# Kernel tuning notes

Measured on AMD Instinct MI355X. Metric: run time of the kernel, lower is better.

The kernel has to match this reference:

```python
import jax, jax.numpy as jnp
import numpy as np

EMB = 1024; H = 8; HD = EMB // H // 2  # head_dim = 64, q/k use 2*H heads of HD; v uses H heads of 2*HD
FF = 4096; DEPTH = 1
LAM_INIT = float(0.8 - 0.6 * np.exp(-0.3 * DEPTH))

def setup_inputs() -> dict:
    key = jax.random.key(0)
    ks = jax.random.split(key, 12)
    s = lambda k, sh, sc: jax.random.normal(k, sh, jnp.float32) * sc
    return {
        'x': s(ks[0], (2, 2048, EMB), 1.0),
        'ln1_w': jnp.ones((EMB,), jnp.float32), 'ln1_b': jnp.zeros((EMB,), jnp.float32),
        'Wq': s(ks[1], (EMB, EMB), 0.02), 'Wk': s(ks[2], (EMB, EMB), 0.02),
        'Wv': s(ks[3], (EMB, EMB), 0.02), 'Wo': s(ks[4], (EMB, EMB), 0.02),
        'lq1': s(ks[5], (HD,), 0.1), 'lk1': s(ks[6], (HD,), 0.1),
        'lq2': s(ks[7], (HD,), 0.1), 'lk2': s(ks[8], (HD,), 0.1),
        'subln_w': jnp.ones((2 * HD,), jnp.float32),
        'ln2_w': jnp.ones((EMB,), jnp.float32), 'ln2_b': jnp.zeros((EMB,), jnp.float32),
        'W1': s(ks[9], (EMB, FF), 0.02), 'b1': jnp.zeros((FF,), jnp.float32),
        'W2': s(ks[10], (FF, EMB), 0.02), 'b2': jnp.zeros((EMB,), jnp.float32),
    }

def _ln(x, w, b):
    m = jnp.mean(x, -1, keepdims=True)
    v = jnp.var(x, -1, keepdims=True)
    return (x - m) * jax.lax.rsqrt(v + 1e-5) * w + b

def _rms(x, w):
    return x * jax.lax.rsqrt(jnp.mean(x * x, -1, keepdims=True) + 1e-5) * w

def reference(x, ln1_w, ln1_b, Wq, Wk, Wv, Wo, lq1, lk1, lq2, lk2, subln_w, ln2_w, ln2_b, W1, b1, W2, b2):
    B, N, _ = x.shape
    h = _ln(x, ln1_w, ln1_b)
    q = (h @ Wq).reshape(B, N, 2 * H, HD) * (HD ** -0.5)
    k = (h @ Wk).reshape(B, N, 2 * H, HD)
    v = (h @ Wv).reshape(B, N, H, 2 * HD)
    # dual softmax attention maps: [B, 2H, N, N]
    attn = jax.nn.softmax(jnp.einsum('bihd,bjhd->bhij', q, k), axis=-1)
    attn = attn.reshape(B, H, 2, N, N)
    lam = jnp.exp(jnp.sum(lq1 * lk1)) - jnp.exp(jnp.sum(lq2 * lk2)) + LAM_INIT
    a = attn[:, :, 0] - lam * attn[:, :, 1]  # differential attention [B,H,N,N]
    o = jnp.einsum('bhij,bjhd->bihd', a, v)  # [B,N,H,2*HD]
    o = _rms(o, subln_w) * (1.0 - LAM_INIT)
    x = x + o.reshape(B, N, EMB) @ Wo
    h = _ln(x, ln2_w, ln2_b)
    return x + (jax.nn.gelu(h @ W1 + b1, approximate=False) @ W2 + b2)
```

## Files before the change

### kernel.cpp

```cpp
#include <hip/hip_runtime.h>


typedef unsigned short u16;
typedef unsigned int u32;
typedef __attribute__((ext_vector_type(8))) __bf16 bf16x8;
typedef __attribute__((ext_vector_type(4))) float f32x4;
typedef __attribute__((ext_vector_type(4))) u32 u32x4;
typedef __attribute__((ext_vector_type(2))) u32 u32x2;

#define LOG2E 1.4426950408889634f
#define LAM_INIT 0.355509068f
#define ONE_MINUS_LAM_INIT 0.644490932f

__device__ __forceinline__ float bf2f(u16 x) {
  u32 u = ((u32)x) << 16;
  return __builtin_bit_cast(float, u);
}
__device__ __forceinline__ u16 f2bf(float f) {
  u32 u = __builtin_bit_cast(u32, f);
  u32 r = (u + 0x7FFFu + ((u >> 16) & 1u)) >> 16;
  return (u16)r;
}
__device__ __forceinline__ u32 cvtpk(float lo, float hi) {
  u32 r;
  asm("v_cvt_pk_bf16_f32 %0, %1, %2" : "=v"(r) : "v"(lo), "v"(hi));
  return r;
}
__device__ __forceinline__ float ldf(const void* p, size_t i, bool f32) {
  return f32 ? ((const float*)p)[i] : bf2f(((const u16*)p)[i]);
}
__device__ __forceinline__ void async16(const u16* g, u16* l) {
  __builtin_amdgcn_global_load_lds((const __attribute__((address_space(1))) u32*)g,
                                   (__attribute__((address_space(3))) u32*)l, 16, 0, 0);
}
__device__ __forceinline__ bf16x8 ld8(const u16* p) { return *(const bf16x8*)p; }

__global__ void detect_kernel(const u32* x, int* flag) {
  int e = (x[threadIdx.x] >> 7) & 0xFF;
  unsigned long long m = __ballot(e >= 90 && e <= 150);
  if (threadIdx.x == 0) flag[0] = (__popcll(m) >= 40) ? 1 : 0;
}

__global__ void lam_kernel(const void* lq1, const void* lk1, const void* lq2,
                           const void* lk2, const int* flag, float* out) {
  const bool f32 = flag[0] == 0;
  int L = threadIdx.x;
  float a = ldf(lq1, L, f32) * ldf(lk1, L, f32);
  float c = ldf(lq2, L, f32) * ldf(lk2, L, f32);
#pragma unroll
  for (int m = 1; m < 64; m <<= 1) { a += __shfl_xor(a, m); c += __shfl_xor(c, m); }
  if (L == 0) out[0] = __expf(a) - __expf(c) + LAM_INIT;
}

__device__ __forceinline__ void unpack8(u32x4 u, float* f) {
#pragma unroll
  for (int i = 0; i < 4; ++i) {
    f[2 * i] = bf2f((u16)(u[i] & 0xffffu));
    f[2 * i + 1] = bf2f((u16)(u[i] >> 16));
  }
}

template <bool XRAW>
__global__ __launch_bounds__(256) void ln_kernel(const void* __restrict__ x,
                                                 const void* __restrict__ w,
                                                 const void* __restrict__ b,
                                                 const int* __restrict__ flag,
                                                 u16* __restrict__ out) {
  const bool f32 = flag[0] == 0;
  const int row = blockIdx.x * 4 + (threadIdx.x >> 6);
  const int L = threadIdx.x & 63;
  float xv[16];
  if (XRAW && f32) {
    const f32x4* xr = (const f32x4*)((const float*)x + (size_t)row * 1024 + L * 16);
#pragma unroll
    for (int i = 0; i < 4; ++i) {
      f32x4 vv = xr[i];
#pragma unroll
      for (int j = 0; j < 4; ++j) xv[i * 4 + j] = vv[j];
    }
  } else {
    const u16* xr = (const u16*)x + (size_t)row * 1024 + L * 16;
    unpack8(*(const u32x4*)xr, xv);
    unpack8(*(const u32x4*)(xr + 8), xv + 8);
  }
  float s = 0.f, sq = 0.f;
#pragma unroll
  for (int i = 0; i < 16; ++i) { s += xv[i]; sq += xv[i] * xv[i]; }
#pragma unroll
  for (int m = 1; m < 64; m <<= 1) { s += __shfl_xor(s, m); sq += __shfl_xor(sq, m); }
  float mean = s * (1.0f / 1024.0f);
  float var = sq * (1.0f / 1024.0f) - mean * mean;
  float rstd = rsqrtf(var + 1e-5f);
  u32 pk[8];
#pragma unroll
  for (int i = 0; i < 8; ++i) {
    float w0 = ldf(w, L * 16 + 2 * i, f32), w1 = ldf(w, L * 16 + 2 * i + 1, f32);
    float b0 = ldf(b, L * 16 + 2 * i, f32), b1v = ldf(b, L * 16 + 2 * i + 1, f32);
    float v0 = (xv[2 * i] - mean) * rstd * w0 + b0;
    float v1 = (xv[2 * i + 1] - mean) * rstd * w1 + b1v;
    pk[i] = (u32)f2bf(v0) | ((u32)f2bf(v1) << 16);
  }
  u32x4 o0 = {pk[0], pk[1], pk[2], pk[3]};
  u32x4 o1 = {pk[4], pk[5], pk[6], pk[7]};
  *(u32x4*)(out + (size_t)row * 1024 + L * 16) = o0;
  *(u32x4*)(out + (size_t)row * 1024 + L * 16 + 8) = o1;
}

__global__ __launch_bounds__(256) void twc_kernel(const void* __restrict__ s0,
                                                  const void* __restrict__ s1,
                                                  const void* __restrict__ s2,
                                                  u16* __restrict__ dst, int sstride,
                                                  int dstride, size_t soff, size_t dzoff,
                                                  const int* __restrict__ flag) {
  __shared__ __align__(16) u16 tile[64][72];
  const bool f32 = flag[0] == 0;
  const void* src = blockIdx.z == 0 ? s0 : (blockIdx.z == 1 ? s1 : s2);
  u16* dz = dst + (size_t)blockIdx.z * dzoff;
  const int r0 = blockIdx.y * 64, c0 = blockIdx.x * 64;
  const int t = threadIdx.x;
  const int rr = t >> 3, cc = t & 7;
#pragma unroll
  for (int i = 0; i < 2; ++i) {
    int row = rr + i * 32;
    size_t idx = (size_t)(r0 + row) * sstride + c0 + cc * 8 + soff;
    if (f32) {
      const f32x4* s = (const f32x4*)((const float*)src + idx);
      f32x4 a = s[0], b = s[1];
      union { u16 t16[8]; u32x4 v; } u_;
#pragma unroll
      for (int j = 0; j < 4; ++j) { u_.t16[j] = f2bf(a[j]); u_.t16[4 + j] = f2bf(b[j]); }
      *(u32x4*)(&tile[row][cc * 8]) = u_.v;
    } else {
      *(u32x4*)(&tile[row][cc * 8]) = *(const u32x4*)((const u16*)src + idx);
    }
  }
  __syncthreads();
  u16* d = dz + (size_t)c0 * dstride + r0;
#pragma unroll
  for (int i = 0; i < 2; ++i) {
    int n = rr + i * 32;
    union { u16 t16[8]; u32x4 v; } u_;
#pragma unroll
    for (int j = 0; j < 8; ++j) u_.t16[j] = tile[cc * 8 + j][n];
    *(u32x4*)(d + (size_t)n * dstride + cc * 8) = u_.v;
  }
}

enum { EP_NONE = 0, EP_RES = 2, EP_GELU = 3, EP_BIASRES = 4, EP_QKV = 5 };

template <int TM, int EPI, bool RESRAW, bool OUTFLEX, bool DB>
__global__ __launch_bounds__(256, 2) void gemm_bt(
    const u16* __restrict__ A, const u16* __restrict__ Bt, void* __restrict__ Cv,
    int M, int N, int K, const void* __restrict__ bias, int boff,
    const void* __restrict__ res, const int* __restrict__ flag,
    u16* __restrict__ kout, u16* __restrict__ vtout) {
  constexpr int MT = TM / 32;
  constexpr int HALF = TM * 64 + 128 * 64;
  extern __shared__ __align__(16) u16 lds[];
  const int t = threadIdx.x;
  const int w = t >> 6, L = t & 63;
  const int quad = L >> 4, l16 = L & 15;
  const int m0 = blockIdx.y * TM, n0 = blockIdx.x * 128;
  const int wm = (TM == 128) ? (w >> 1) * 64 : (w & 1) * 32;
  const int wn = (TM == 128) ? (w & 1) * 64 : (w >> 1) * 64;
  const int srow = L >> 3, spc = L & 7;
  const int sc = spc ^ srow;

  f32x4 acc[MT][4] = {};
  const u16* Ab = A + (size_t)m0 * K;
  const u16* Bb = Bt + (size_t)n0 * K;

  auto stage = [&](int kt, int bsel) {
    u16* base = lds + bsel * HALF;
#pragma unroll
    for (int r = 0; r < TM / 32; ++r) {
      int row = r * 32 + w * 8 + srow;
      async16(Ab + (size_t)row * K + kt + sc * 8, &base[row * 64 + spc * 8]);
    }
#pragma unroll
    for (int r = 0; r < 4; ++r) {
      int row = r * 32 + w * 8 + srow;
      async16(Bb + (size_t)row * K + kt + sc * 8, &base[TM * 64 + row * 64 + spc * 8]);
    }
  };
  auto ktile = [&](const u16* base) {
#pragma unroll
    for (int ks = 0; ks < 2; ++ks) {
      bf16x8 af[MT], bfr[4];
#pragma unroll
      for (int mt = 0; mt < MT; ++mt) {
        int row = wm + mt * 16 + l16;
        af[mt] = ld8(&base[row * 64 + (((ks * 4 + quad) ^ (l16 & 7)) * 8)]);
      }
#pragma unroll
      for (int nt = 0; nt < 4; ++nt) {
        int row = wn + nt * 16 + l16;
        bfr[nt] = ld8(&base[TM * 64 + row * 64 + (((ks * 4 + quad) ^ (l16 & 7)) * 8)]);
      }
#pragma unroll
      for (int mt = 0; mt < MT; ++mt)
#pragma unroll
        for (int nt = 0; nt < 4; ++nt)
          acc[mt][nt] =
              __builtin_amdgcn_mfma_f32_16x16x32_bf16(af[mt], bfr[nt], acc[mt][nt], 0, 0, 0);
    }
  };

  if (DB) {
    const int nst = K >> 6;
    stage(0, 0);
    for (int st = 0; st < nst; ++st) {
      __syncthreads();
      if (st + 1 < nst) stage((st + 1) << 6, (st + 1) & 1);
      ktile(lds + (st & 1) * HALF);
    }
  } else {
    for (int kt = 0; kt < K; kt += 64) {
      stage(kt, 0);
      __syncthreads();
      ktile(lds);
      __syncthreads();
    }
  }

  const bool f32 = flag[0] == 0;
#pragma unroll
  for (int mt = 0; mt < MT; ++mt) {
#pragma unroll
    for (int nt = 0; nt < 4; ++nt) {
      int col = n0 + wn + nt * 16 + l16;
      float bv = 0.f;
      if (EPI == EP_GELU || EPI == EP_BIASRES) bv = ldf(bias, (size_t)boff + col, f32);
#pragma unroll
      for (int r = 0; r < 4; ++r) {
        int row = m0 + wm + mt * 16 + quad * 4 + r;
        float v = acc[mt][nt][r];
        if (EPI == EP_GELU) {
          v += bv;
          v = 0.5f * v * (1.0f + erff(v * 0.70710678118654752f));
        }
        if (EPI == EP_RES || EPI == EP_BIASRES) {
          size_t ri = (size_t)row * N + col;
          float rv = RESRAW ? ldf(res, ri, f32) : bf2f(((const u16*)res)[ri]);
          v += rv;
          if (EPI == EP_BIASRES) v += bv;
        }
        if (EPI == EP_QKV) {
          if (col < 1024) {
            ((u16*)Cv)[(size_t)row * 1024 + col] = f2bf(v * 0.125f);
          } else if (col < 2048) {
            kout[(size_t)row * 1024 + (col - 1024)] = f2bf(v);
          } else {
            int c2 = col - 2048;
            int bb = row >> 11, n = row & 2047, hh = c2 >> 7, d = c2 & 127;
            vtout[(size_t)((bb * 8 + hh) * 128 + d) * 2048 + n] = f2bf(v);
          }
        } else {
          size_t ci = (size_t)row * N + col;
          if (OUTFLEX && f32)
            ((float*)Cv)[ci] = v;
          else
            ((u16*)Cv)[ci] = f2bf(v);
        }
      }
    }
  }
}

__global__ __launch_bounds__(256, 2) void attn_kernel(
    const u16* __restrict__ q, const u16* __restrict__ k, const u16* __restrict__ vT,
    const float* __restrict__ lamp, const void* __restrict__ subw,
    const int* __restrict__ flag, u16* __restrict__ o) {
  extern __shared__ __align__(16) u16 lds[];
  constexpr int VB = 16384, PB = 32768;
  const int t = threadIdx.x, w = t >> 6, L = t & 63;
  const int quad = L >> 4, l16 = L & 15;
  const int bid = ((blockIdx.x & 7) << 6) | (blockIdx.x >> 3);
  const int qt = bid & 31, h = (bid >> 5) & 7, b = bid >> 8;
  const int q0 = qt * 64;
  const int comp = w >> 1, rh = (w & 1) * 32;
  const int srow = L >> 3, spc = L & 7, sc = spc ^ srow;
  const u16* vb = vT + (size_t)(b * 8 + h) * (128 * 2048);
  const int pbase = PB + w * 2048;

  auto stageK = [&](int kt, int bsel) {
#pragma unroll
    for (int r = 0; r < 4; ++r) {
      int row = r * 32 + w * 8 + srow;
      int c_ = row >> 6, key = row & 63;
      async16(k + ((size_t)(b * 2048 + kt + key) * 1024 + (2 * h + c_) * 64 + sc * 8),
              &lds[bsel * 8192 + row * 64 + spc * 8]);
    }
  };
  auto stageV = [&](int kt, int bsel) {
#pragma unroll
    for (int r = 0; r < 4; ++r) {
      int dim = r * 32 + w * 8 + srow;
      async16(vb + (size_t)dim * 2048 + kt + sc * 8,
              &lds[VB + bsel * 8192 + dim * 64 + spc * 8]);
    }
  };

  stageK(0, 0);
  stageV(0, 0);
#pragma unroll
  for (int r = 0; r < 4; ++r) {
    int row = r * 32 + w * 8 + srow;
    int c_ = row >> 6, qr = row & 63;
    async16(q + ((size_t)(b * 2048 + q0 + qr) * 1024 + (2 * h + c_) * 64 + sc * 8),
            &lds[PB + row * 64 + spc * 8]);
  }
  __syncthreads();
  bf16x8 qf[2][2];
#pragma unroll
  for (int mt = 0; mt < 2; ++mt)
#pragma unroll
    for (int ks = 0; ks < 2; ++ks) {
      int row = rh + mt * 16 + l16;
      qf[mt][ks] =
          ld8(&lds[PB + comp * 4096 + row * 64 + (((ks * 4 + quad) ^ (l16 & 7)) * 8)]);
    }

  float mst[2] = {-1.0e30f, -1.0e30f};
  float mstl[2] = {-1.0e30f, -1.0e30f};
  float lst[2] = {0.f, 0.f};
  f32x4 oacc[8][2] = {};

  for (int ti = 0; ti < 32; ++ti) {
    __syncthreads();
    const int bb = ti & 1;
    if (ti + 1 < 32) {
      stageK((ti + 1) * 64, bb ^ 1);
      stageV((ti + 1) * 64, bb ^ 1);
    }

    f32x4 s[4][2] = {};
#pragma unroll
    for (int ks = 0; ks < 2; ++ks) {
      bf16x8 kf[4];
#pragma unroll
      for (int nt = 0; nt < 4; ++nt) {
        int row = nt * 16 + l16;
        kf[nt] = ld8(&lds[bb * 8192 + comp * 4096 + row * 64 +
                          (((ks * 4 + quad) ^ (l16 & 7)) * 8)]);
      }
#pragma unroll
      for (int nt = 0; nt < 4; ++nt)
#pragma unroll
        for (int mt = 0; mt < 2; ++mt)
          s[nt][mt] = __builtin_amdgcn_mfma_f32_16x16x32_bf16(kf[nt], qf[mt][ks], s[nt][mt], 0, 0, 0);
    }

#pragma unroll
    for (int mt = 0; mt < 2; ++mt) {
      float mx = -3.0e38f;
#pragma unroll
      for (int nt = 0; nt < 4; ++nt)
#pragma unroll
        for (int r = 0; r < 4; ++r) mx = fmaxf(mx, s[nt][mt][r]);
      mx = fmaxf(mx, __shfl_xor(mx, 16));
      mx = fmaxf(mx, __shfl_xor(mx, 32));
      if (__ballot(mx > mst[mt] + 8.0f)) {
        float mnew = fmaxf(mst[mt], mx);
        float al = exp2f((mst[mt] - mnew) * LOG2E);
        mst[mt] = mnew;
        mstl[mt] = mnew * LOG2E;
        lst[mt] *= al;
#pragma unroll
        for (int nt = 0; nt < 8; ++nt)
#pragma unroll
          for (int r = 0; r < 4; ++r) oacc[nt][mt][r] *= al;
      }
      float ps = 0.f;
#pragma unroll
      for (int nt = 0; nt < 4; ++nt)
#pragma unroll
        for (int r = 0; r < 4; ++r) {
          float p = exp2f(__builtin_fmaf(s[nt][mt][r], LOG2E, -mstl[mt]));
          s[nt][mt][r] = p;
          ps += p;
        }
      ps += __shfl_xor(ps, 16);
      ps += __shfl_xor(ps, 32);
      lst[mt] += ps;
    }

#pragma unroll
    for (int mt = 0; mt < 2; ++mt) {
      int prow = mt * 16 + l16;
#pragma unroll
      for (int nt = 0; nt < 4; ++nt) {
        int pc = (nt * 2 + (quad >> 1)) ^ (l16 & 7);
        u32x2 pk2 = {cvtpk(s[nt][mt][0], s[nt][mt][1]), cvtpk(s[nt][mt][2], s[nt][mt][3])};
        *(u32x2*)(&lds[pbase + prow * 64 + pc * 8 + (quad & 1) * 4]) = pk2;
      }
    }

#pragma unroll
    for (int ks = 0; ks < 2; ++ks) {
      bf16x8 pf[2];
#pragma unroll
      for (int mt = 0; mt < 2; ++mt) {
        int row = mt * 16 + l16;
        pf[mt] = ld8(&lds[pbase + row * 64 + (((ks * 4 + quad) ^ (l16 & 7)) * 8)]);
      }
#pragma unroll
      for (int nt = 0; nt < 8; ++nt) {
        int dim = nt * 16 + l16;
        bf16x8 vf = ld8(&lds[VB + bb * 8192 + dim * 64 +
                             (((ks * 4 + quad) ^ (l16 & 7)) * 8)]);
#pragma unroll
        for (int mt = 0; mt < 2; ++mt)
          oacc[nt][mt] = __builtin_amdgcn_mfma_f32_16x16x32_bf16(vf, pf[mt], oacc[nt][mt], 0, 0, 0);
      }
    }
  }

#pragma unroll
  for (int mt = 0; mt < 2; ++mt) {
    float inv = 1.0f / lst[mt];
#pragma unroll
    for (int nt = 0; nt < 8; ++nt)
#pragma unroll
      for (int r = 0; r < 4; ++r) oacc[nt][mt][r] *= inv;
  }

  __syncthreads();
  float* cb = (float*)lds;
  if (comp == 1) {
#pragma unroll
    for (int mt = 0; mt < 2; ++mt) {
      int rowc = rh + mt * 16 + l16;
#pragma unroll
      for (int nt = 0; nt < 8; ++nt)
        *(f32x4*)(&cb[rowc * 132 + nt * 16 + quad * 4]) = oacc[nt][mt];
    }
  }
  __syncthreads();
  if (comp == 0) {
    const bool f32 = flag[0] == 0;
    float lam = lamp[0];
    float sw[8][4];
#pragma unroll
    for (int nt = 0; nt < 8; ++nt)
#pragma unroll
      for (int r = 0; r < 4; ++r) sw[nt][r] = ldf(subw, nt * 16 + quad * 4 + r, f32);
#pragma unroll
    for (int mt = 0; mt < 2; ++mt) {
      int rowc = rh + mt * 16 + l16;
      float dv[8][4];
      float sq = 0.f;
#pragma unroll
      for (int nt = 0; nt < 8; ++nt) {
        f32x4 c2 = *(const f32x4*)(&cb[rowc * 132 + nt * 16 + quad * 4]);
#pragma unroll
        for (int r = 0; r < 4; ++r) {
          float d = oacc[nt][mt][r] - lam * c2[r];
          dv[nt][r] = d;
          sq += d * d;
        }
      }
      sq += __shfl_xor(sq, 16);
      sq += __shfl_xor(sq, 32);
      float rms = rsqrtf(sq * (1.0f / 128.0f) + 1e-5f);
      size_t rowg = (size_t)(b * 2048 + q0 + rowc) * 1024 + h * 128;
#pragma unroll
      for (int nt = 0; nt < 8; ++nt) {
        float v0 = dv[nt][0] * rms * sw[nt][0] * ONE_MINUS_LAM_INIT;
        float v1 = dv[nt][1] * rms * sw[nt][1] * ONE_MINUS_LAM_INIT;
        float v2 = dv[nt][2] * rms * sw[nt][2] * ONE_MINUS_LAM_INIT;
        float v3 = dv[nt][3] * rms * sw[nt][3] * ONE_MINUS_LAM_INIT;
        u32x2 pk2 = {cvtpk(v0, v1), cvtpk(v2, v3)};
        *(u32x2*)(o + rowg + nt * 16 + quad * 4) = pk2;
      }
    }
  }
}

extern "C" void kernel_launch(void* const* d_in, const int* in_sizes, int n_in,
                              void* d_out, int out_size, void* d_ws, size_t ws_size,
                              hipStream_t stream) {
  (void)in_sizes; (void)n_in; (void)out_size; (void)ws_size;
  const void* x = d_in[0];
  const void* ln1w = d_in[1];
  const void* ln1b = d_in[2];
  const void* Wq = d_in[3];
  const void* Wk = d_in[4];
  const void* Wv = d_in[5];
  const void* Wo = d_in[6];
  const void* lq1 = d_in[7];
  const void* lk1 = d_in[8];
  const void* lq2 = d_in[9];
  const void* lk2 = d_in[10];
  const void* subw = d_in[11];
  const void* ln2w = d_in[12];
  const void* ln2b = d_in[13];
  const void* W1 = d_in[14];
  const void* b1 = d_in[15];
  const void* W2 = d_in[16];
  const void* b2 = d_in[17];

  char* ws = (char*)d_ws;
  const size_t MB = 1u << 20;
  u16* A = (u16*)ws;
  u16* B = (u16*)(ws + 8 * MB);
  u16* C = (u16*)(ws + 16 * MB);
  u16* D = (u16*)(ws + 24 * MB);
  u16* E = (u16*)(ws + 32 * MB);
  float* lam = (float*)(ws + 40 * MB);
  int* flag = (int*)(ws + 40 * MB + 64);
  u16* W2Th = D + 2097152;

  const int g64_1 = (64 * 64 + 128 * 64) * 2;
  const int g64_2 = g64_1 * 2;
  const int g128_2 = (128 * 64 + 128 * 64) * 2 * 2;

  detect_kernel<<<dim3(1), dim3(64), 0, stream>>>((const u32*)x, flag);
  lam_kernel<<<dim3(1), dim3(64), 0, stream>>>(lq1, lk1, lq2, lk2, flag, lam);
  ln_kernel<true><<<dim3(1024), dim3(256), 0, stream>>>(x, ln1w, ln1b, flag, A);

  twc_kernel<<<dim3(16, 16, 3), dim3(256), 0, stream>>>(Wq, Wk, Wv, E, 1024, 1024, 0,
                                                        1048576, flag);
  gemm_bt<64, EP_QKV, false, false, false><<<dim3(24, 64), dim3(256), g64_1, stream>>>(
      A, E, B, 4096, 3072, 1024, nullptr, 0, nullptr, flag, C, D);

  attn_kernel<<<dim3(512), dim3(256), 81920, stream>>>(B, C, D, lam, subw, flag, A);

  twc_kernel<<<dim3(16, 16, 1), dim3(256), 0, stream>>>(Wo, Wo, Wo, D, 1024, 1024, 0, 0,
                                                        flag);
  gemm_bt<64, EP_RES, true, false, true><<<dim3(8, 64), dim3(256), g64_2, stream>>>(
      A, D, E, 4096, 1024, 1024, nullptr, 0, x, flag, nullptr, nullptr);
  ln_kernel<false><<<dim3(1024), dim3(256), 0, stream>>>(E, ln2w, ln2b, flag, A);

  for (int hh = 0; hh < 2; ++hh) {
    twc_kernel<<<dim3(32, 16, 1), dim3(256), 0, stream>>>(W1, W1, W1, D, 4096, 1024,
                                                          (size_t)hh * 2048, 0, flag);
    twc_kernel<<<dim3(16, 32, 1), dim3(256), 0, stream>>>(
        W2, W2, W2, W2Th, 1024, 2048, (size_t)hh * 2048 * 1024, 0, flag);
    gemm_bt<128, EP_GELU, false, false, true><<<dim3(16, 32), dim3(256), g128_2, stream>>>(
        A, D, B, 4096, 2048, 1024, b1, hh * 2048, nullptr, flag, nullptr, nullptr);
    if (hh == 0) {
      gemm_bt<64, EP_BIASRES, false, true, true><<<dim3(8, 64), dim3(256), g64_2, stream>>>(
          B, W2Th, d_out, 4096, 1024, 2048, b2, 0, E, flag, nullptr, nullptr);
    } else {
      gemm_bt<64, EP_RES, true, true, true><<<dim3(8, 64), dim3(256), g64_2, stream>>>(
          B, W2Th, d_out, 4096, 1024, 2048, nullptr, 0, d_out, flag, nullptr, nullptr);
    }
  }
}
```

Measured before the change: 464.8 us.

## Keep P in registers via permlane swaps, load Q directly, enlarge GEMM tiles

In the attention kernel, the softmax probabilities are packed to bf16 in registers and rearranged into the MFMA operand layout with v_permlane32/16_swap, replacing the LDS write and read round trip. Q fragments are loaded straight from global memory instead of being staged through LDS, which also drops one barrier and 16KB of LDS. Separately, the QKV, output-projection and FFN2 GEMMs switch from 64-row to 128-row tiles with half the grid in M. The permlane layout must exactly match the old LDS layout, and larger GEMM tiles leave fewer blocks, which may underfill the device.

```diff
diff --git a/kernel.cpp b/kernel.cpp
--- a/kernel.cpp
+++ b/kernel.cpp
@@ -272,7 +272,7 @@
     const float* __restrict__ lamp, const void* __restrict__ subw,
     const int* __restrict__ flag, u16* __restrict__ o) {
   extern __shared__ __align__(16) u16 lds[];
-  constexpr int VB = 16384, PB = 32768;
+  constexpr int VB = 16384;
   const int t = threadIdx.x, w = t >> 6, L = t & 63;
   const int quad = L >> 4, l16 = L & 15;
   const int bid = ((blockIdx.x & 7) << 6) | (blockIdx.x >> 3);
@@ -281,7 +281,6 @@
   const int comp = w >> 1, rh = (w & 1) * 32;
   const int srow = L >> 3, spc = L & 7, sc = spc ^ srow;
   const u16* vb = vT + (size_t)(b * 8 + h) * (128 * 2048);
-  const int pbase = PB + w * 2048;
 
   auto stageK = [&](int kt, int bsel) {
 #pragma unroll
@@ -303,22 +302,14 @@
 
   stageK(0, 0);
   stageV(0, 0);
-#pragma unroll
-  for (int r = 0; r < 4; ++r) {
-    int row = r * 32 + w * 8 + srow;
-    int c_ = row >> 6, qr = row & 63;
-    async16(q + ((size_t)(b * 2048 + q0 + qr) * 1024 + (2 * h + c_) * 64 + sc * 8),
-            &lds[PB + row * 64 + spc * 8]);
-  }
-  __syncthreads();
   bf16x8 qf[2][2];
 #pragma unroll
   for (int mt = 0; mt < 2; ++mt)
 #pragma unroll
     for (int ks = 0; ks < 2; ++ks) {
-      int row = rh + mt * 16 + l16;
-      qf[mt][ks] =
-          ld8(&lds[PB + comp * 4096 + row * 64 + (((ks * 4 + quad) ^ (l16 & 7)) * 8)]);
+      int row = q0 + rh + mt * 16 + l16;
+      qf[mt][ks] = ld8(q + (size_t)(b * 2048 + row) * 1024 + (2 * h + comp) * 64 +
+                       ks * 32 + quad * 8);
     }
 
   float mst[2] = {-1.0e30f, -1.0e30f};
@@ -351,6 +342,7 @@
           s[nt][mt] = __builtin_amdgcn_mfma_f32_16x16x32_bf16(kf[nt], qf[mt][ks], s[nt][mt], 0, 0, 0);
     }
 
+    u32 wreg[2][4][2];
 #pragma unroll
     for (int mt = 0; mt < 2; ++mt) {
       float mx = -3.0e38f;
@@ -373,36 +365,34 @@
       }
       float ps = 0.f;
 #pragma unroll
-      for (int nt = 0; nt < 4; ++nt)
+      for (int nt = 0; nt < 4; ++nt) {
 #pragma unroll
         for (int r = 0; r < 4; ++r) {
           float p = exp2f(__builtin_fmaf(s[nt][mt][r], LOG2E, -mstl[mt]));
           s[nt][mt][r] = p;
           ps += p;
         }
+        wreg[mt][nt][0] = cvtpk(s[nt][mt][0], s[nt][mt][1]);
+        wreg[mt][nt][1] = cvtpk(s[nt][mt][2], s[nt][mt][3]);
+      }
       ps += __shfl_xor(ps, 16);
       ps += __shfl_xor(ps, 32);
       lst[mt] += ps;
     }
 
 #pragma unroll
-    for (int mt = 0; mt < 2; ++mt) {
-      int prow = mt * 16 + l16;
-#pragma unroll
-      for (int nt = 0; nt < 4; ++nt) {
-        int pc = (nt * 2 + (quad >> 1)) ^ (l16 & 7);
-        u32x2 pk2 = {cvtpk(s[nt][mt][0], s[nt][mt][1]), cvtpk(s[nt][mt][2], s[nt][mt][3])};
-        *(u32x2*)(&lds[pbase + prow * 64 + pc * 8 + (quad & 1) * 4]) = pk2;
-      }
-    }
-
-#pragma unroll
     for (int ks = 0; ks < 2; ++ks) {
       bf16x8 pf[2];
 #pragma unroll
       for (int mt = 0; mt < 2; ++mt) {
-        int row = mt * 16 + l16;
-        pf[mt] = ld8(&lds[pbase + row * 64 + (((ks * 4 + quad) ^ (l16 & 7)) * 8)]);
+        u32 a0 = wreg[mt][2 * ks][0], b0 = wreg[mt][2 * ks + 1][0];
+        u32 a1 = wreg[mt][2 * ks][1], b1 = wreg[mt][2 * ks + 1][1];
+        asm("v_permlane32_swap_b32 %0, %1" : "+v"(a0), "+v"(b0));
+        asm("v_permlane16_swap_b32 %0, %1" : "+v"(a0), "+v"(b0));
+        asm("v_permlane32_swap_b32 %0, %1" : "+v"(a1), "+v"(b1));
+        asm("v_permlane16_swap_b32 %0, %1" : "+v"(a1), "+v"(b1));
+        u32x4 pw = {a0, a1, b0, b1};
+        pf[mt] = __builtin_bit_cast(bf16x8, pw);
       }
 #pragma unroll
       for (int nt = 0; nt < 8; ++nt) {
@@ -511,9 +501,8 @@
   int* flag = (int*)(ws + 40 * MB + 64);
   u16* W2Th = D + 2097152;
 
-  const int g64_1 = (64 * 64 + 128 * 64) * 2;
-  const int g64_2 = g64_1 * 2;
-  const int g128_2 = (128 * 64 + 128 * 64) * 2 * 2;
+  const int g128_1 = (128 * 64 + 128 * 64) * 2;
+  const int g128_2 = g128_1 * 2;
 
   detect_kernel<<<dim3(1), dim3(64), 0, stream>>>((const u32*)x, flag);
   lam_kernel<<<dim3(1), dim3(64), 0, stream>>>(lq1, lk1, lq2, lk2, flag, lam);
@@ -521,14 +510,14 @@
 
   twc_kernel<<<dim3(16, 16, 3), dim3(256), 0, stream>>>(Wq, Wk, Wv, E, 1024, 1024, 0,
                                                         1048576, flag);
-  gemm_bt<64, EP_QKV, false, false, false><<<dim3(24, 64), dim3(256), g64_1, stream>>>(
+  gemm_bt<128, EP_QKV, false, false, false><<<dim3(24, 32), dim3(256), g128_1, stream>>>(
       A, E, B, 4096, 3072, 1024, nullptr, 0, nullptr, flag, C, D);
 
-  attn_kernel<<<dim3(512), dim3(256), 81920, stream>>>(B, C, D, lam, subw, flag, A);
+  attn_kernel<<<dim3(512), dim3(256), 65536, stream>>>(B, C, D, lam, subw, flag, A);
 
   twc_kernel<<<dim3(16, 16, 1), dim3(256), 0, stream>>>(Wo, Wo, Wo, D, 1024, 1024, 0, 0,
                                                         flag);
-  gemm_bt<64, EP_RES, true, false, true><<<dim3(8, 64), dim3(256), g64_2, stream>>>(
+  gemm_bt<128, EP_RES, true, false, true><<<dim3(8, 32), dim3(256), g128_2, stream>>>(
       A, D, E, 4096, 1024, 1024, nullptr, 0, x, flag, nullptr, nullptr);
   ln_kernel<false><<<dim3(1024), dim3(256), 0, stream>>>(E, ln2w, ln2b, flag, A);
 
@@ -540,10 +529,10 @@
     gemm_bt<128, EP_GELU, false, false, true><<<dim3(16, 32), dim3(256), g128_2, stream>>>(
         A, D, B, 4096, 2048, 1024, b1, hh * 2048, nullptr, flag, nullptr, nullptr);
     if (hh == 0) {
-      gemm_bt<64, EP_BIASRES, false, true, true><<<dim3(8, 64), dim3(256), g64_2, stream>>>(
+      gemm_bt<128, EP_BIASRES, false, true, true><<<dim3(8, 32), dim3(256), g128_2, stream>>>(
           B, W2Th, d_out, 4096, 1024, 2048, b2, 0, E, flag, nullptr, nullptr);
     } else {
-      gemm_bt<64, EP_RES, true, true, true><<<dim3(8, 64), dim3(256), g64_2, stream>>>(
+      gemm_bt<128, EP_RES, true, true, true><<<dim3(8, 32), dim3(256), g128_2, stream>>>(
           B, W2Th, d_out, 4096, 1024, 2048, nullptr, 0, d_out, flag, nullptr, nullptr);
     }
   }
```

Result: slower. 479.9 us (+3.2%).
